# Kernel tuning notes

Measured on AMD Instinct MI355X. Metric: run time of the kernel, lower is better.

## Reference

```python
import jax, jax.numpy as jnp
import numpy as np

B, S, D, H, C = 64, 512, 768, 768, 5


def setup_inputs() -> dict:
    key = jax.random.key(0)
    ks = jax.random.split(key, 7)
    return {
        "hidden_states": jax.random.normal(ks[0], (B, S, D), jnp.float32),
        "mask": jnp.ones((B, S), dtype=bool),
        # Dense(hidden_size, relu)
        "W1": jax.random.normal(ks[1], (D, H), jnp.float32) * 0.02,
        "b1": jnp.zeros((H,), jnp.float32),
        # CRF inner dense -> potentials over num_classes
        "W2": jax.random.normal(ks[2], (H, C), jnp.float32) * 0.02,
        "b2": jnp.zeros((C,), jnp.float32),
        # CRF transition matrix and boundary energies (tfa use_boundary=True)
        "chain_kernel": jax.random.normal(ks[3], (C, C), jnp.float32) * 0.1,
        "left_boundary": jax.random.normal(ks[4], (C,), jnp.float32) * 0.1,
        "right_boundary": jax.random.normal(ks[5], (C,), jnp.float32) * 0.1,
    }


def viterbi_decode(potentials, trans):
    """potentials: [B,S,C], trans: [C,C] -> decoded tags [B,S] int32."""
    pot_t = jnp.swapaxes(potentials, 0, 1)  # [S,B,C]

    def fwd_step(alpha, pot):
        scores = alpha[:, :, None] + trans[None]      # [B,C_prev,C_cur]
        bp = jnp.argmax(scores, axis=1)               # [B,C]
        alpha = jnp.max(scores, axis=1) + pot         # [B,C]
        return alpha, bp

    alpha, bps = jax.lax.scan(fwd_step, pot_t[0], pot_t[1:])  # bps: [S-1,B,C]
    last = jnp.argmax(alpha, axis=-1).astype(jnp.int32)       # [B]

    def back_step(tag, bp):
        prev = jnp.take_along_axis(bp, tag[:, None], axis=1)[:, 0].astype(jnp.int32)
        return prev, prev

    _, tags = jax.lax.scan(back_step, last, bps, reverse=True)  # [S-1,B]
    decoded = jnp.concatenate([jnp.swapaxes(tags, 0, 1), last[:, None]], axis=1)
    return decoded


def reference(hidden_states, mask, W1, b1, W2, b2, chain_kernel,
              left_boundary, right_boundary):
    # Dense + ReLU (dropout is identity at inference / training=False)
    h = jax.nn.relu(jnp.einsum('bsd,dh->bsh', hidden_states, W1) + b1)
    # CRF inner dense -> unary potentials
    pot = jnp.einsum('bsh,hc->bsc', h, W2) + b2
    # boundary energies at first / last timestep (mask is full-length here)
    pot = pot.at[:, 0].add(left_boundary).at[:, -1].add(right_boundary)
    seq_length = jnp.sum(mask.astype(jnp.int32), axis=1)
    decoded = viterbi_decode(pot, chain_kernel)
    return decoded, pot, seq_length, chain_kernel
```

## Files before the change

kernel.cpp:

```cpp
#include <hip/hip_runtime.h>

#define B_  64
#define S_  512
#define D_  768
#define H_  768
#define C_  5
#define M_  (B_ * S_)

typedef float f32x4 __attribute__((ext_vector_type(4)));
typedef short short8 __attribute__((ext_vector_type(8)));

#define W1T_ELEMS (D_ * H_)
#define XBF_ELEMS (M_ * D_)

#define PX_BLOCKS   (XBF_ELEMS / (256 * 8))
#define PW_BLOCKS   ((D_ / 32) * (H_ / 32))
#define PI_BLOCKS   ((M_ * C_ + 255) / 256)

__device__ __forceinline__ unsigned short f2bf(float f) {
    unsigned int u = __float_as_uint(f);
    u += 0x7FFFu + ((u >> 16) & 1u);
    return (unsigned short)(u >> 16);
}

__global__ __launch_bounds__(256) void prep_all_kernel(
    const float* __restrict__ X, const float* __restrict__ W1,
    const float* __restrict__ b2, const float* __restrict__ lb,
    const float* __restrict__ rb,
    unsigned short* __restrict__ xbf, unsigned short* __restrict__ w1t,
    float* __restrict__ pot)
{
    __shared__ float t[32][33];
    const int bid = blockIdx.x;
    const int tid = threadIdx.x;

    if (bid < PX_BLOCKS) {
        const size_t i0 = ((size_t)bid * 256 + tid) * 8;
        const float4 a = *(const float4*)(X + i0);
        const float4 b = *(const float4*)(X + i0 + 4);
        union { unsigned short u[8]; uint4 v; } o;
        o.u[0] = f2bf(a.x); o.u[1] = f2bf(a.y); o.u[2] = f2bf(a.z); o.u[3] = f2bf(a.w);
        o.u[4] = f2bf(b.x); o.u[5] = f2bf(b.y); o.u[6] = f2bf(b.z); o.u[7] = f2bf(b.w);
        *(uint4*)(xbf + i0) = o.v;
    } else if (bid < PX_BLOCKS + PW_BLOCKS) {
        const int b2i = bid - PX_BLOCKS;
        const int bx = b2i % (H_ / 32);
        const int by = b2i / (H_ / 32);
        const int lx = tid & 31, ly = tid >> 5;
        #pragma unroll
        for (int j = 0; j < 4; ++j)
            t[ly + 8 * j][lx] = W1[(by * 32 + ly + 8 * j) * H_ + bx * 32 + lx];
        __syncthreads();
        #pragma unroll
        for (int j = 0; j < 4; ++j)
            w1t[(size_t)(bx * 32 + ly + 8 * j) * D_ + by * 32 + lx] = f2bf(t[lx][ly + 8 * j]);
    } else {
        const int idx = (bid - PX_BLOCKS - PW_BLOCKS) * 256 + tid;
        if (idx < M_ * C_) {
            const int c = idx % C_;
            const int tt = (idx / C_) & (S_ - 1);
            float v = b2[c];
            if (tt == 0)      v += lb[c];
            if (tt == S_ - 1) v += rb[c];
            pot[idx] = v;
        }
    }
}

__global__ __launch_bounds__(256) void prep_w1_kernel(
    const float* __restrict__ W1, unsigned short* __restrict__ w1t)
{
    __shared__ float t[32][33];
    const int bx = blockIdx.x, by = blockIdx.y;
    const int lx = threadIdx.x & 31, ly = threadIdx.x >> 5;
    #pragma unroll
    for (int j = 0; j < 4; ++j)
        t[ly + 8 * j][lx] = W1[(by * 32 + ly + 8 * j) * H_ + bx * 32 + lx];
    __syncthreads();
    #pragma unroll
    for (int j = 0; j < 4; ++j)
        w1t[(size_t)(bx * 32 + ly + 8 * j) * D_ + by * 32 + lx] = f2bf(t[lx][ly + 8 * j]);
}

__global__ __launch_bounds__(256) void init_pot_kernel(
    const float* __restrict__ b2, const float* __restrict__ lb,
    const float* __restrict__ rb, float* __restrict__ pot)
{
    const int idx = blockIdx.x * 256 + threadIdx.x;
    if (idx < M_ * C_) {
        const int c = idx % C_;
        const int t = (idx / C_) & (S_ - 1);
        float v = b2[c];
        if (t == 0)      v += lb[c];
        if (t == S_ - 1) v += rb[c];
        pot[idx] = v;
    }
}

__device__ __forceinline__ void gload16(const void* g, void* l) {
    __builtin_amdgcn_global_load_lds(
        (const __attribute__((address_space(1))) unsigned int*)g,
        (__attribute__((address_space(3))) unsigned int*)l, 16, 0, 0);
}

__global__ __launch_bounds__(256) void gemm_bk64_kernel(
    const unsigned short* __restrict__ xbf,
    const unsigned short* __restrict__ w1t,
    const float* __restrict__ b1,
    const float* __restrict__ W2,
    float* __restrict__ pot)
{
    __shared__ __align__(16) unsigned short Asm[2][8192];
    __shared__ __align__(16) unsigned short Bsm[2][8192];

    const int tid  = threadIdx.x;
    const int lane = tid & 63, w = tid >> 6;
    const int wm   = w >> 1, wn = w & 1;
    const int i15  = lane & 15, quad = lane >> 4;

    const int bid = blockIdx.x;
    const int r8 = bid & 7, q8 = bid >> 3;
    const int nb = q8 % 6, mhi = q8 / 6;
    const int m0 = (mhi * 8 + r8) * 128;
    const int n0 = nb * 128;

    const unsigned short* gA[2];
    const unsigned short* gB[2];
    int lofs[2];
    #pragma unroll
    for (int i = 0; i < 2; ++i) {
        const int g = 2 * w + i;
        gA[i] = xbf + (size_t)(m0 + g * 16 + i15) * D_ + quad * 8;
        gB[i] = w1t + (size_t)(n0 + g * 16 + i15) * D_ + quad * 8;
        lofs[i] = g * 512;
    }

    f32x4 acc[4][4];
    #pragma unroll
    for (int mi = 0; mi < 4; ++mi)
        #pragma unroll
        for (int ni = 0; ni < 4; ++ni)
            acc[mi][ni] = (f32x4){0.f, 0.f, 0.f, 0.f};

    #pragma unroll
    for (int i = 0; i < 2; ++i) {
        gload16(gA[i],      &Asm[0][lofs[i]]);
        gload16(gA[i] + 32, &Asm[0][4096 + lofs[i]]);
        gload16(gB[i],      &Bsm[0][lofs[i]]);
        gload16(gB[i] + 32, &Bsm[0][4096 + lofs[i]]);
        gA[i] += 64; gB[i] += 64;
    }
    __syncthreads();

    #define KITERS (D_ / 64)
    for (int kt = 0; kt < KITERS; ++kt) {
        const int cur = kt & 1, nxt = cur ^ 1;

        if (kt + 1 < KITERS) {
            #pragma unroll
            for (int i = 0; i < 2; ++i) {
                gload16(gA[i],      &Asm[nxt][lofs[i]]);
                gload16(gA[i] + 32, &Asm[nxt][4096 + lofs[i]]);
                gload16(gB[i],      &Bsm[nxt][lofs[i]]);
                gload16(gB[i] + 32, &Bsm[nxt][4096 + lofs[i]]);
                gA[i] += 64; gB[i] += 64;
            }
        }

        #pragma unroll
        for (int c = 0; c < 2; ++c) {
            const int cb = c * 4096;
            short8 af[4], bfr[4];
            #pragma unroll
            for (int mi = 0; mi < 4; ++mi)
                af[mi] = *(const short8*)&Asm[cur][cb + (wm * 4 + mi) * 512 + quad * 128 + i15 * 8];
            #pragma unroll
            for (int ni = 0; ni < 4; ++ni)
                bfr[ni] = *(const short8*)&Bsm[cur][cb + (wn * 4 + ni) * 512 + quad * 128 + i15 * 8];
            #pragma unroll
            for (int ni = 0; ni < 4; ++ni)
                #pragma unroll
                for (int mi = 0; mi < 4; ++mi)
                    acc[mi][ni] = __builtin_amdgcn_mfma_f32_16x16x32_bf16(
                        af[mi], bfr[ni], acc[mi][ni], 0, 0, 0);
        }

        __syncthreads();
    }

    float* pp = (float*)&Asm[0][0];

    float b1v[4], w2v[4][C_];
    #pragma unroll
    for (int ni = 0; ni < 4; ++ni) {
        const int col = n0 + wn * 64 + ni * 16 + i15;
        b1v[ni] = b1[col];
        #pragma unroll
        for (int cc = 0; cc < C_; ++cc) w2v[ni][cc] = W2[col * C_ + cc];
    }

    #pragma unroll
    for (int mi = 0; mi < 4; ++mi) {
        float ps[4][C_];
        #pragma unroll
        for (int r = 0; r < 4; ++r)
            #pragma unroll
            for (int cc = 0; cc < C_; ++cc) ps[r][cc] = 0.f;

        #pragma unroll
        for (int ni = 0; ni < 4; ++ni)
            #pragma unroll
            for (int r = 0; r < 4; ++r) {
                float h = acc[mi][ni][r] + b1v[ni];
                h = h > 0.f ? h : 0.f;
                #pragma unroll
                for (int cc = 0; cc < C_; ++cc)
                    ps[r][cc] = fmaf(h, w2v[ni][cc], ps[r][cc]);
            }

        #pragma unroll
        for (int off = 1; off < 16; off <<= 1)
            #pragma unroll
            for (int r = 0; r < 4; ++r)
                #pragma unroll
                for (int cc = 0; cc < C_; ++cc)
                    ps[r][cc] += __shfl_xor(ps[r][cc], off, 64);

        if (i15 == 0) {
            #pragma unroll
            for (int r = 0; r < 4; ++r) {
                const int row = wm * 64 + mi * 16 + quad * 4 + r;
                #pragma unroll
                for (int cc = 0; cc < C_; ++cc)
                    pp[(wn * 128 + row) * C_ + cc] = ps[r][cc];
            }
        }
    }
    __syncthreads();

    for (int idx = tid; idx < 128 * C_; idx += 256) {
        const int row = idx / C_, cc = idx % C_;
        atomicAdd(&pot[(size_t)(m0 + row) * C_ + cc],
                  pp[row * C_ + cc] + pp[(128 + row) * C_ + cc]);
    }
}

__global__ __launch_bounds__(256) void gemm_bf16_kernel(
    const float* __restrict__ X,
    const unsigned short* __restrict__ w1t,
    const float* __restrict__ b1,
    const float* __restrict__ W2,
    float* __restrict__ pot)
{
    __shared__ __align__(16) float          Asm[128 * 32];
    __shared__ __align__(16) unsigned short Bsm[128 * 32];
    __shared__ float pp[2][128][C_];

    const int tid  = threadIdx.x;
    const int lane = tid & 63, w = tid >> 6;
    const int wm   = w >> 1, wn = w & 1;
    const int i15  = lane & 15, quad = lane >> 4;

    const int bid = blockIdx.x;
    const int r8 = bid & 7, q8 = bid >> 3;
    const int nb = q8 % 6, mhi = q8 / 6;
    const int m0 = (mhi * 8 + r8) * 128;
    const int n0 = nb * 128;

    const float* gA[4];
    float* lA[4];
    const unsigned short* gB[2];
    unsigned short* lB[2];
    #pragma unroll
    for (int i = 0; i < 4; ++i) {
        const int a = 4 * w + i, g = a >> 1, h = a & 1;
        gA[i] = X + (size_t)(m0 + g * 16 + i15) * D_ + (4 * h + quad) * 4;
        lA[i] = &Asm[g * 512 + h * 256];
    }
    #pragma unroll
    for (int i = 0; i < 2; ++i) {
        const int b = 2 * w + i;
        gB[i] = w1t + (size_t)(n0 + b * 16 + i15) * D_ + quad * 8;
        lB[i] = &Bsm[b * 512];
    }

    f32x4 acc[4][4];
    #pragma unroll
    for (int mi = 0; mi < 4; ++mi)
        #pragma unroll
        for (int ni = 0; ni < 4; ++ni)
            acc[mi][ni] = (f32x4){0.f, 0.f, 0.f, 0.f};

    for (int kt = 0; kt < D_ / 32; ++kt) {
        __syncthreads();
        #pragma unroll
        for (int i = 0; i < 4; ++i) { gload16(gA[i], lA[i]); gA[i] += 32; }
        #pragma unroll
        for (int i = 0; i < 2; ++i) { gload16(gB[i], lB[i]); gB[i] += 32; }
        __syncthreads();

        short8 af[4];
        #pragma unroll
        for (int mi = 0; mi < 4; ++mi) {
            const int row = wm * 64 + mi * 16 + i15;
            const int base = (row >> 4) * 512 + (row & 15) * 4 + quad * 128;
            const f32x4 lo = *(const f32x4*)&Asm[base];
            const f32x4 hi = *(const f32x4*)&Asm[base + 64];
            float f[8];
            *(f32x4*)&f[0] = lo; *(f32x4*)&f[4] = hi;
            union { short8 s; unsigned short u[8]; } cv;
            #pragma unroll
            for (int j = 0; j < 8; ++j) cv.u[j] = f2bf(f[j]);
            af[mi] = cv.s;
        }
        short8 bfr[4];
        #pragma unroll
        for (int ni = 0; ni < 4; ++ni) {
            const int row = wn * 64 + ni * 16 + i15;
            bfr[ni] = *(const short8*)&Bsm[(row >> 4) * 512 + quad * 128 + (row & 15) * 8];
        }
        #pragma unroll
        for (int ni = 0; ni < 4; ++ni)
            #pragma unroll
            for (int mi = 0; mi < 4; ++mi)
                acc[mi][ni] = __builtin_amdgcn_mfma_f32_16x16x32_bf16(
                    af[mi], bfr[ni], acc[mi][ni], 0, 0, 0);
    }

    float b1v[4], w2v[4][C_];
    #pragma unroll
    for (int ni = 0; ni < 4; ++ni) {
        const int col = n0 + wn * 64 + ni * 16 + i15;
        b1v[ni] = b1[col];
        #pragma unroll
        for (int cc = 0; cc < C_; ++cc) w2v[ni][cc] = W2[col * C_ + cc];
    }

    #pragma unroll
    for (int mi = 0; mi < 4; ++mi) {
        float ps[4][C_];
        #pragma unroll
        for (int r = 0; r < 4; ++r)
            #pragma unroll
            for (int cc = 0; cc < C_; ++cc) ps[r][cc] = 0.f;

        #pragma unroll
        for (int ni = 0; ni < 4; ++ni)
            #pragma unroll
            for (int r = 0; r < 4; ++r) {
                float h = acc[mi][ni][r] + b1v[ni];
                h = h > 0.f ? h : 0.f;
                #pragma unroll
                for (int cc = 0; cc < C_; ++cc)
                    ps[r][cc] = fmaf(h, w2v[ni][cc], ps[r][cc]);
            }

        #pragma unroll
        for (int off = 1; off < 16; off <<= 1)
            #pragma unroll
            for (int r = 0; r < 4; ++r)
                #pragma unroll
                for (int cc = 0; cc < C_; ++cc)
                    ps[r][cc] += __shfl_xor(ps[r][cc], off, 64);

        if (i15 == 0) {
            #pragma unroll
            for (int r = 0; r < 4; ++r) {
                const int row = wm * 64 + mi * 16 + quad * 4 + r;
                #pragma unroll
                for (int cc = 0; cc < C_; ++cc)
                    pp[wn][row][cc] = ps[r][cc];
            }
        }
    }
    __syncthreads();

    for (int idx = tid; idx < 128 * C_; idx += 256) {
        const int row = idx / C_, cc = idx % C_;
        atomicAdd(&pot[(size_t)(m0 + row) * C_ + cc],
                  pp[0][row][cc] + pp[1][row][cc]);
    }
}

#define FBK 8
#define FLDS 132
__global__ __launch_bounds__(256) void gemm_relu_pot_kernel(
    const float* __restrict__ X, const float* __restrict__ W1,
    const float* __restrict__ b1, const float* __restrict__ W2,
    float* __restrict__ pot)
{
    __shared__ float As[FBK * FLDS];
    __shared__ float Bs[FBK * FLDS];
    __shared__ float w2s[128][C_];

    const int tid = threadIdx.x;
    const int tx = tid & 15, ty = tid >> 4;
    const int m0 = blockIdx.y * 128, n0 = blockIdx.x * 128;

    for (int idx = tid; idx < 128 * C_; idx += 256)
        w2s[idx / C_][idx % C_] = W2[(n0 + idx / C_) * C_ + idx % C_];

    float acc[2][2][4][4];
    #pragma unroll
    for (int a = 0; a < 2; ++a)
        #pragma unroll
        for (int b = 0; b < 2; ++b)
            #pragma unroll
            for (int i = 0; i < 4; ++i)
                #pragma unroll
                for (int j = 0; j < 4; ++j) acc[a][b][i][j] = 0.f;

    const int arow = tid >> 1, aq = tid & 1;
    const int brow = tid >> 5, bq = tid & 31;
    const float* Aptr = X + (m0 + arow) * D_ + aq * 4;
    const float* Bptr = W1 + brow * H_ + n0 + bq * 4;

    for (int kt = 0; kt < D_; kt += FBK) {
        const float4 avv = *(const float4*)Aptr;
        const float4 bvv = *(const float4*)Bptr;
        __syncthreads();
        As[(aq * 4 + 0) * FLDS + arow] = avv.x;
        As[(aq * 4 + 1) * FLDS + arow] = avv.y;
        As[(aq * 4 + 2) * FLDS + arow] = avv.z;
        As[(aq * 4 + 3) * FLDS + arow] = avv.w;
        *(float4*)&Bs[brow * FLDS + bq * 4] = bvv;
        __syncthreads();
        #pragma unroll
        for (int k = 0; k < FBK; ++k) {
            const float4 a0 = *(const float4*)&As[k * FLDS + (ty << 2)];
            const float4 a1 = *(const float4*)&As[k * FLDS + 64 + (ty << 2)];
            const float4 b0 = *(const float4*)&Bs[k * FLDS + (tx << 2)];
            const float4 b1r = *(const float4*)&Bs[k * FLDS + 64 + (tx << 2)];
            const float ar[2][4] = {{a0.x,a0.y,a0.z,a0.w},{a1.x,a1.y,a1.z,a1.w}};
            const float br[2][4] = {{b0.x,b0.y,b0.z,b0.w},{b1r.x,b1r.y,b1r.z,b1r.w}};
            #pragma unroll
            for (int ri = 0; ri < 2; ++ri)
                #pragma unroll
                for (int i = 0; i < 4; ++i)
                    #pragma unroll
                    for (int rj = 0; rj < 2; ++rj)
                        #pragma unroll
                        for (int j = 0; j < 4; ++j)
                            acc[ri][rj][i][j] = fmaf(ar[ri][i], br[rj][j], acc[ri][rj][i][j]);
        }
        Aptr += FBK;
        Bptr += FBK * H_;
    }

    float ps[2][4][C_];
    #pragma unroll
    for (int ri = 0; ri < 2; ++ri)
        #pragma unroll
        for (int i = 0; i < 4; ++i)
            #pragma unroll
            for (int cc = 0; cc < C_; ++cc) ps[ri][i][cc] = 0.f;

    #pragma unroll
    for (int rj = 0; rj < 2; ++rj)
        #pragma unroll
        for (int j = 0; j < 4; ++j) {
            const int nl = rj * 64 + (tx << 2) + j;
            const float bj = b1[n0 + nl];
            float w2c[C_];
            #pragma unroll
            for (int cc = 0; cc < C_; ++cc) w2c[cc] = w2s[nl][cc];
            #pragma unroll
            for (int ri = 0; ri < 2; ++ri)
                #pragma unroll
                for (int i = 0; i < 4; ++i) {
                    float h = acc[ri][rj][i][j] + bj;
                    h = h > 0.f ? h : 0.f;
                    #pragma unroll
                    for (int cc = 0; cc < C_; ++cc)
                        ps[ri][i][cc] = fmaf(h, w2c[cc], ps[ri][i][cc]);
                }
        }

    #pragma unroll
    for (int off = 1; off < 16; off <<= 1)
        #pragma unroll
        for (int ri = 0; ri < 2; ++ri)
            #pragma unroll
            for (int i = 0; i < 4; ++i)
                #pragma unroll
                for (int cc = 0; cc < C_; ++cc)
                    ps[ri][i][cc] += __shfl_xor(ps[ri][i][cc], off, 64);

    if (tx == 0)
        #pragma unroll
        for (int ri = 0; ri < 2; ++ri)
            #pragma unroll
            for (int i = 0; i < 4; ++i) {
                const int m = m0 + ri * 64 + (ty << 2) + i;
                #pragma unroll
                for (int cc = 0; cc < C_; ++cc)
                    atomicAdd(&pot[m * C_ + cc], ps[ri][i][cc]);
            }
}

__global__ __launch_bounds__(64) void viterbi_kernel(
    const float* __restrict__ pot, const float* __restrict__ trans,
    const int* __restrict__ mask, float* __restrict__ decoded,
    float* __restrict__ seqlen, float* __restrict__ chain_out)
{
    const int b = blockIdx.x;
    const int lane = threadIdx.x;

    __shared__ float pl[S_ * C_];
    __shared__ unsigned int bpk[S_];
    __shared__ unsigned int gseg[64];
    __shared__ int bt[64];
    __shared__ int dec_s[S_];
    __shared__ int s_last;

    const float* pb = pot + b * (S_ * C_);
    for (int i = lane; i < S_ * C_; i += 64) pl[i] = pb[i];

    int mcnt = 0;
    const int* mb = mask + b * S_;
    for (int i = lane; i < S_; i += 64) mcnt += (mb[i] != 0) ? 1 : 0;
    #pragma unroll
    for (int off = 32; off >= 1; off >>= 1) mcnt += __shfl_xor(mcnt, off, 64);

    if (b == 0 && lane < C_ * C_) chain_out[lane] = trans[lane];

    float tr[C_][C_];
    #pragma unroll
    for (int p = 0; p < C_; ++p)
        #pragma unroll
        for (int c = 0; c < C_; ++c) tr[p][c] = trans[p * C_ + c];

    __syncthreads();

    const float NEG = -1.0e30f;

    float G[C_][C_];
    #pragma unroll
    for (int c = 0; c < C_; ++c)
        #pragma unroll
        for (int p = 0; p < C_; ++p) G[c][p] = (c == p) ? 0.f : NEG;

    for (int j = 1; j <= 8; ++j) {
        const int t = 8 * lane + j;
        if (t < S_) {
            float ng[C_][C_];
            #pragma unroll
            for (int c = 0; c < C_; ++c) {
                const float pc = pl[t * C_ + c];
                #pragma unroll
                for (int p = 0; p < C_; ++p) {
                    float m = tr[0][c] + G[0][p];
                    #pragma unroll
                    for (int q = 1; q < C_; ++q)
                        m = fmaxf(m, tr[q][c] + G[q][p]);
                    ng[c][p] = m + pc;
                }
            }
            #pragma unroll
            for (int c = 0; c < C_; ++c)
                #pragma unroll
                for (int p = 0; p < C_; ++p) G[c][p] = ng[c][p];
        }
    }

    #pragma unroll
    for (int d = 1; d < 64; d <<= 1) {
        float Q[C_][C_];
        #pragma unroll
        for (int q = 0; q < C_; ++q)
            #pragma unroll
            for (int p = 0; p < C_; ++p) Q[q][p] = __shfl_up(G[q][p], d, 64);
        if (lane >= d) {
            float ng[C_][C_];
            #pragma unroll
            for (int c = 0; c < C_; ++c)
                #pragma unroll
                for (int p = 0; p < C_; ++p) {
                    float m = G[c][0] + Q[0][p];
                    #pragma unroll
                    for (int q = 1; q < C_; ++q)
                        m = fmaxf(m, G[c][q] + Q[q][p]);
                    ng[c][p] = m;
                }
            #pragma unroll
            for (int c = 0; c < C_; ++c)
                #pragma unroll
                for (int p = 0; p < C_; ++p) G[c][p] = ng[c][p];
        }
    }

    float a[C_];
    {
        float E[C_][C_];
        #pragma unroll
        for (int c = 0; c < C_; ++c)
            #pragma unroll
            for (int p = 0; p < C_; ++p) E[c][p] = __shfl_up(G[c][p], 1, 64);
        float a0[C_];
        #pragma unroll
        for (int c = 0; c < C_; ++c) a0[c] = pl[c];
        if (lane == 0) {
            #pragma unroll
            for (int c = 0; c < C_; ++c) a[c] = a0[c];
        } else {
            #pragma unroll
            for (int c = 0; c < C_; ++c) {
                float m = E[c][0] + a0[0];
                #pragma unroll
                for (int q = 1; q < C_; ++q) m = fmaxf(m, E[c][q] + a0[q]);
                a[c] = m;
            }
        }
    }

    for (int j = 1; j <= 8; ++j) {
        const int t = 8 * lane + j;
        if (t < S_) {
            unsigned int mpack = 0;
            float na[C_];
            #pragma unroll
            for (int c = 0; c < C_; ++c) {
                float best = a[0] + tr[0][c];
                int arg = 0;
                #pragma unroll
                for (int p = 1; p < C_; ++p) {
                    const float s = a[p] + tr[p][c];
                    if (s > best) { best = s; arg = p; }
                }
                mpack |= (unsigned int)arg << (3 * c);
                na[c] = best + pl[t * C_ + c];
            }
            bpk[t] = mpack;
            #pragma unroll
            for (int c = 0; c < C_; ++c) a[c] = na[c];
        }
    }

    if (lane == 63) {
        float best = a[0];
        int arg = 0;
        #pragma unroll
        for (int p = 1; p < C_; ++p)
            if (a[p] > best) { best = a[p]; arg = p; }
        s_last = arg;
    }
    if (lane == 0) bpk[0] = 0;
    __syncthreads();

    const int last = s_last;

    unsigned int g = 0u | (1u << 3) | (2u << 6) | (3u << 9) | (4u << 12);
    #pragma unroll
    for (int j = 7; j >= 0; --j) {
        const int t = 8 * lane + j;
        if (t >= 1) {
            const unsigned int m = bpk[t];
            unsigned int ng = 0;
            #pragma unroll
            for (int x = 0; x < C_; ++x) {
                const unsigned int gx = (g >> (3 * x)) & 7u;
                ng |= ((m >> (3 * gx)) & 7u) << (3 * x);
            }
            g = ng;
        }
    }
    gseg[lane] = g;
    __syncthreads();

    if (lane == 0) {
        int cur = last;
        for (int l = 63; l >= 0; --l) {
            bt[l] = cur;
            cur = (int)((gseg[l] >> (3 * cur)) & 7u);
        }
        seqlen[b] = (float)mcnt;
    }
    __syncthreads();

    {
        int tag = bt[lane];
        const int t0 = 8 * lane;
        dec_s[t0 + 7] = tag;
        #pragma unroll
        for (int t = t0 + 7; t >= t0 + 1; --t) {
            tag = (int)((bpk[t] >> (3 * tag)) & 7u);
            dec_s[t - 1] = tag;
        }
    }
    __syncthreads();

    float* db = decoded + b * S_;
    for (int i = lane; i < S_; i += 64) db[i] = (float)dec_s[i];
}

extern "C" void kernel_launch(void* const* d_in, const int* in_sizes, int n_in,
                              void* d_out, int out_size, void* d_ws, size_t ws_size,
                              hipStream_t stream) {
    const float* hs    = (const float*)d_in[0];
    const int*   mask  = (const int*)  d_in[1];
    const float* W1    = (const float*)d_in[2];
    const float* b1    = (const float*)d_in[3];
    const float* W2    = (const float*)d_in[4];
    const float* b2    = (const float*)d_in[5];
    const float* chain = (const float*)d_in[6];
    const float* lb    = (const float*)d_in[7];
    const float* rb    = (const float*)d_in[8];

    float* out      = (float*)d_out;
    float* decoded  = out;
    float* pot      = out + M_;
    float* seq      = out + M_ + M_ * C_;
    float* chainout = seq + B_;

    const size_t need_w1 = (size_t)W1T_ELEMS * sizeof(unsigned short);
    const size_t need_all = need_w1 + (size_t)XBF_ELEMS * sizeof(unsigned short);

    if (ws_size >= need_all) {
        unsigned short* w1t = (unsigned short*)d_ws;
        unsigned short* xbf = w1t + W1T_ELEMS;
        prep_all_kernel<<<PX_BLOCKS + PW_BLOCKS + PI_BLOCKS, 256, 0, stream>>>(
            hs, W1, b2, lb, rb, xbf, w1t, pot);
        gemm_bk64_kernel<<<1536, 256, 0, stream>>>(xbf, w1t, b1, W2, pot);
    } else if (ws_size >= need_w1) {
        unsigned short* w1t = (unsigned short*)d_ws;
        init_pot_kernel<<<PI_BLOCKS, 256, 0, stream>>>(b2, lb, rb, pot);
        dim3 pgrid(H_ / 32, D_ / 32);
        prep_w1_kernel<<<pgrid, 256, 0, stream>>>(W1, w1t);
        gemm_bf16_kernel<<<1536, 256, 0, stream>>>(hs, w1t, b1, W2, pot);
    } else {
        init_pot_kernel<<<PI_BLOCKS, 256, 0, stream>>>(b2, lb, rb, pot);
        dim3 grid(H_ / 128, M_ / 128);
        gemm_relu_pot_kernel<<<grid, 256, 0, stream>>>(hs, W1, b1, W2, pot);
    }

    viterbi_kernel<<<B_, 64, 0, stream>>>(pot, chain, mask, decoded, seq, chainout);
}
```

Before: 272.9 us.

## Warp-specialize GEMM into producer/consumer waves with LDS ring buffer

Replaces the double-buffered BK=64 GEMM with a warp-specialized kernel. Two extra producer waves stream A and B tiles into a 3-deep LDS ring using async global-to-LDS loads, and four consumer waves run MFMA, synchronised through per-slot ready/consumed counters in LDS instead of block-wide barriers. The aim is to overlap loads with compute without __syncthreads stalls each k-step. In exchange it adds spin-wait overhead, a 384-thread block size and a smaller K tile (32), and it changes the block-to-tile mapping, dropping the grouped swizzle, which may hurt L2 reuse.

```diff
diff --git a/kernel.cpp b/kernel.cpp
--- a/kernel.cpp
+++ b/kernel.cpp
@@ -103,145 +103,165 @@
         (__attribute__((address_space(3))) unsigned int*)l, 16, 0, 0);
 }
 
-__global__ __launch_bounds__(256) void gemm_bk64_kernel(
+#define RING 3
+#define KTILES (D_ / 32)
+
+__global__ __launch_bounds__(384) void gemm_pc_kernel(
     const unsigned short* __restrict__ xbf,
     const unsigned short* __restrict__ w1t,
     const float* __restrict__ b1,
     const float* __restrict__ W2,
     float* __restrict__ pot)
 {
-    __shared__ __align__(16) unsigned short Asm[2][8192];
-    __shared__ __align__(16) unsigned short Bsm[2][8192];
+    __shared__ __align__(16) unsigned short Asl[RING][4096];
+    __shared__ __align__(16) unsigned short Bsl[RING][4096];
+    __shared__ int ready[RING];
+    __shared__ int consumed[RING];
 
     const int tid  = threadIdx.x;
     const int lane = tid & 63, w = tid >> 6;
-    const int wm   = w >> 1, wn = w & 1;
     const int i15  = lane & 15, quad = lane >> 4;
 
     const int bid = blockIdx.x;
-    const int r8 = bid & 7, q8 = bid >> 3;
-    const int nb = q8 % 6, mhi = q8 / 6;
-    const int m0 = (mhi * 8 + r8) * 128;
+    const int mt = bid / 6, nb = bid % 6;
+    const int m0 = mt * 128;
     const int n0 = nb * 128;
 
-    const unsigned short* gA[2];
-    const unsigned short* gB[2];
-    int lofs[2];
-    #pragma unroll
-    for (int i = 0; i < 2; ++i) {
-        const int g = 2 * w + i;
-        gA[i] = xbf + (size_t)(m0 + g * 16 + i15) * D_ + quad * 8;
-        gB[i] = w1t + (size_t)(n0 + g * 16 + i15) * D_ + quad * 8;
-        lofs[i] = g * 512;
-    }
-
-    f32x4 acc[4][4];
-    #pragma unroll
-    for (int mi = 0; mi < 4; ++mi)
-        #pragma unroll
-        for (int ni = 0; ni < 4; ++ni)
-            acc[mi][ni] = (f32x4){0.f, 0.f, 0.f, 0.f};
-
-    #pragma unroll
-    for (int i = 0; i < 2; ++i) {
-        gload16(gA[i],      &Asm[0][lofs[i]]);
-        gload16(gA[i] + 32, &Asm[0][4096 + lofs[i]]);
-        gload16(gB[i],      &Bsm[0][lofs[i]]);
-        gload16(gB[i] + 32, &Bsm[0][4096 + lofs[i]]);
-        gA[i] += 64; gB[i] += 64;
-    }
+    if (tid < RING) { ready[tid] = 0; consumed[tid] = 0; }
     __syncthreads();
 
-    #define KITERS (D_ / 64)
-    for (int kt = 0; kt < KITERS; ++kt) {
-        const int cur = kt & 1, nxt = cur ^ 1;
-
-        if (kt + 1 < KITERS) {
-            #pragma unroll
-            for (int i = 0; i < 2; ++i) {
-                gload16(gA[i],      &Asm[nxt][lofs[i]]);
-                gload16(gA[i] + 32, &Asm[nxt][4096 + lofs[i]]);
-                gload16(gB[i],      &Bsm[nxt][lofs[i]]);
-                gload16(gB[i] + 32, &Bsm[nxt][4096 + lofs[i]]);
-                gA[i] += 64; gB[i] += 64;
-            }
-        }
-
-        #pragma unroll
-        for (int c = 0; c < 2; ++c) {
-            const int cb = c * 4096;
+    float* ppal = (float*)&Asl[0][0];
+
+    if (w >= 4) {
+        const unsigned short* base = (w == 4)
+            ? xbf + (size_t)m0 * D_
+            : w1t + (size_t)n0 * D_;
+        unsigned short* slab = (w == 4) ? &Asl[0][0] : &Bsl[0][0];
+        const size_t lofs = (size_t)i15 * D_ + quad * 8;
+
+        for (int k = 0; k < KTILES; ++k) {
+            const int s = k % RING;
+            if (k >= RING) {
+                const int wantc = 4 * (k / RING);
+                while (__hip_atomic_load(&consumed[s], __ATOMIC_ACQUIRE,
+                                         __HIP_MEMORY_SCOPE_WORKGROUP) < wantc)
+                    __builtin_amdgcn_s_sleep(1);
+            }
+            const unsigned short* src = base + (size_t)k * 32 + lofs;
+            unsigned short* dst = slab + s * 4096;
+            #pragma unroll
+            for (int g = 0; g < 8; ++g)
+                gload16(src + (size_t)(g * 16) * D_, dst + g * 512);
+
+            if (k >= 2) {
+                asm volatile("s_waitcnt vmcnt(16)" ::: "memory");
+                if (lane == 0)
+                    __hip_atomic_fetch_add(&ready[(k - 2) % RING], 1,
+                                           __ATOMIC_RELEASE, __HIP_MEMORY_SCOPE_WORKGROUP);
+            }
+        }
+        asm volatile("s_waitcnt vmcnt(8)" ::: "memory");
+        if (lane == 0)
+            __hip_atomic_fetch_add(&ready[(KTILES - 2) % RING], 1,
+                                   __ATOMIC_RELEASE, __HIP_MEMORY_SCOPE_WORKGROUP);
+        asm volatile("s_waitcnt vmcnt(0)" ::: "memory");
+        if (lane == 0)
+            __hip_atomic_fetch_add(&ready[(KTILES - 1) % RING], 1,
+                                   __ATOMIC_RELEASE, __HIP_MEMORY_SCOPE_WORKGROUP);
+        __syncthreads();
+        __syncthreads();
+    } else {
+        const int wm = w >> 1, wn = w & 1;
+
+        f32x4 acc[4][4];
+        #pragma unroll
+        for (int mi = 0; mi < 4; ++mi)
+            #pragma unroll
+            for (int ni = 0; ni < 4; ++ni)
+                acc[mi][ni] = (f32x4){0.f, 0.f, 0.f, 0.f};
+
+        for (int k = 0; k < KTILES; ++k) {
+            const int s = k % RING;
+            const int want = 2 * (k / RING + 1);
+            while (__hip_atomic_load(&ready[s], __ATOMIC_ACQUIRE,
+                                     __HIP_MEMORY_SCOPE_WORKGROUP) < want)
+                __builtin_amdgcn_s_sleep(1);
+
             short8 af[4], bfr[4];
             #pragma unroll
             for (int mi = 0; mi < 4; ++mi)
-                af[mi] = *(const short8*)&Asm[cur][cb + (wm * 4 + mi) * 512 + quad * 128 + i15 * 8];
+                af[mi] = *(const short8*)&Asl[s][(wm * 4 + mi) * 512 + quad * 128 + i15 * 8];
             #pragma unroll
             for (int ni = 0; ni < 4; ++ni)
-                bfr[ni] = *(const short8*)&Bsm[cur][cb + (wn * 4 + ni) * 512 + quad * 128 + i15 * 8];
+                bfr[ni] = *(const short8*)&Bsl[s][(wn * 4 + ni) * 512 + quad * 128 + i15 * 8];
+
             #pragma unroll
             for (int ni = 0; ni < 4; ++ni)
                 #pragma unroll
                 for (int mi = 0; mi < 4; ++mi)
                     acc[mi][ni] = __builtin_amdgcn_mfma_f32_16x16x32_bf16(
                         af[mi], bfr[ni], acc[mi][ni], 0, 0, 0);
-        }
-
-        __syncthreads();
-    }
-
-    float* pp = (float*)&Asm[0][0];
-
-    float b1v[4], w2v[4][C_];
-    #pragma unroll
-    for (int ni = 0; ni < 4; ++ni) {
-        const int col = n0 + wn * 64 + ni * 16 + i15;
-        b1v[ni] = b1[col];
-        #pragma unroll
-        for (int cc = 0; cc < C_; ++cc) w2v[ni][cc] = W2[col * C_ + cc];
-    }
-
-    #pragma unroll
-    for (int mi = 0; mi < 4; ++mi) {
-        float ps[4][C_];
-        #pragma unroll
-        for (int r = 0; r < 4; ++r)
-            #pragma unroll
-            for (int cc = 0; cc < C_; ++cc) ps[r][cc] = 0.f;
-
-        #pragma unroll
-        for (int ni = 0; ni < 4; ++ni)
-            #pragma unroll
-            for (int r = 0; r < 4; ++r) {
-                float h = acc[mi][ni][r] + b1v[ni];
-                h = h > 0.f ? h : 0.f;
-                #pragma unroll
-                for (int cc = 0; cc < C_; ++cc)
-                    ps[r][cc] = fmaf(h, w2v[ni][cc], ps[r][cc]);
-            }
-
-        #pragma unroll
-        for (int off = 1; off < 16; off <<= 1)
+
+            if (lane == 0)
+                __hip_atomic_fetch_add(&consumed[s], 1,
+                                       __ATOMIC_RELEASE, __HIP_MEMORY_SCOPE_WORKGROUP);
+        }
+
+        __syncthreads();
+
+        float b1v[4], w2v[4][C_];
+        #pragma unroll
+        for (int ni = 0; ni < 4; ++ni) {
+            const int col = n0 + wn * 64 + ni * 16 + i15;
+            b1v[ni] = b1[col];
+            #pragma unroll
+            for (int cc = 0; cc < C_; ++cc) w2v[ni][cc] = W2[col * C_ + cc];
+        }
+
+        #pragma unroll
+        for (int mi = 0; mi < 4; ++mi) {
+            float ps[4][C_];
             #pragma unroll
             for (int r = 0; r < 4; ++r)
                 #pragma unroll
-                for (int cc = 0; cc < C_; ++cc)
-                    ps[r][cc] += __shfl_xor(ps[r][cc], off, 64);
-
-        if (i15 == 0) {
-            #pragma unroll
-            for (int r = 0; r < 4; ++r) {
-                const int row = wm * 64 + mi * 16 + quad * 4 + r;
-                #pragma unroll
-                for (int cc = 0; cc < C_; ++cc)
-                    pp[(wn * 128 + row) * C_ + cc] = ps[r][cc];
-            }
-        }
-    }
-    __syncthreads();
-
-    for (int idx = tid; idx < 128 * C_; idx += 256) {
+                for (int cc = 0; cc < C_; ++cc) ps[r][cc] = 0.f;
+
+            #pragma unroll
+            for (int ni = 0; ni < 4; ++ni)
+                #pragma unroll
+                for (int r = 0; r < 4; ++r) {
+                    float h = acc[mi][ni][r] + b1v[ni];
+                    h = h > 0.f ? h : 0.f;
+                    #pragma unroll
+                    for (int cc = 0; cc < C_; ++cc)
+                        ps[r][cc] = fmaf(h, w2v[ni][cc], ps[r][cc]);
+                }
+
+            #pragma unroll
+            for (int off = 1; off < 16; off <<= 1)
+                #pragma unroll
+                for (int r = 0; r < 4; ++r)
+                    #pragma unroll
+                    for (int cc = 0; cc < C_; ++cc)
+                        ps[r][cc] += __shfl_xor(ps[r][cc], off, 64);
+
+            if (i15 == 0) {
+                #pragma unroll
+                for (int r = 0; r < 4; ++r) {
+                    const int row = wm * 64 + mi * 16 + quad * 4 + r;
+                    #pragma unroll
+                    for (int cc = 0; cc < C_; ++cc)
+                        ppal[(wn * 128 + row) * C_ + cc] = ps[r][cc];
+                }
+            }
+        }
+        __syncthreads();
+    }
+
+    for (int idx = tid; idx < 128 * C_; idx += 384) {
         const int row = idx / C_, cc = idx % C_;
         atomicAdd(&pot[(size_t)(m0 + row) * C_ + cc],
-                  pp[row * C_ + cc] + pp[(128 + row) * C_ + cc]);
+                  ppal[row * C_ + cc] + ppal[(128 + row) * C_ + cc]);
     }
 }
 
@@ -262,9 +282,8 @@
     const int i15  = lane & 15, quad = lane >> 4;
 
     const int bid = blockIdx.x;
-    const int r8 = bid & 7, q8 = bid >> 3;
-    const int nb = q8 % 6, mhi = q8 / 6;
-    const int m0 = (mhi * 8 + r8) * 128;
+    const int mt = bid / 6, nb = bid % 6;
+    const int m0 = mt * 128;
     const int n0 = nb * 128;
 
     const float* gA[4];
@@ -720,7 +739,7 @@
         unsigned short* xbf = w1t + W1T_ELEMS;
         prep_all_kernel<<<PX_BLOCKS + PW_BLOCKS + PI_BLOCKS, 256, 0, stream>>>(
             hs, W1, b2, lb, rb, xbf, w1t, pot);
-        gemm_bk64_kernel<<<1536, 256, 0, stream>>>(xbf, w1t, b1, W2, pot);
+        gemm_pc_kernel<<<1536, 384, 0, stream>>>(xbf, w1t, b1, W2, pot);
     } else if (ws_size >= need_w1) {
         unsigned short* w1t = (unsigned short*)d_ws;
         init_pot_kernel<<<PI_BLOCKS, 256, 0, stream>>>(b2, lb, rb, pot);
```

Result: slower. 357.7 us (+31.1%).
